# Performance work log

Hardware: AMD Instinct MI355X
Metric: run time of the kernel (lower is better)

The kernel has to match this reference:

```python
import jax, jax.numpy as jnp
import numpy as np
import math

H = 512        # hidden_dim
DEPTH = 5
KS = 3         # kernel size
DELTA = 0.1
M = 104        # timestamp == seq_len
NC = 5
B = 512
BN_EPS = 1e-5


def setup_inputs() -> dict:
    key = jax.random.key(0)
    ks = jax.random.split(key, 16)
    inp = {}
    inp['x'] = jax.random.normal(ks[0], (B, 1, M), dtype=jnp.float32)
    # CausalCNN: depth conv layers (first is 1->H, rest H->H), each followed by BN
    inp['conv_w0'] = jax.random.normal(ks[1], (H, 1, KS), dtype=jnp.float32) * (1.0 / np.sqrt(KS))
    inp['conv_b0'] = jnp.zeros((H,), jnp.float32)
    inp['conv_w'] = jax.random.normal(ks[2], (DEPTH - 1, H, H, KS), dtype=jnp.float32) * (1.0 / np.sqrt(H * KS))
    inp['conv_b'] = jnp.zeros((DEPTH - 1, H), jnp.float32)
    inp['bn_gamma'] = jnp.ones((DEPTH, H), jnp.float32)
    inp['bn_beta'] = jnp.zeros((DEPTH, H), jnp.float32)
    # input_proj
    inp['proj_w'] = jax.random.normal(ks[3], (H, H), dtype=jnp.float32) * (1.0 / np.sqrt(H))
    inp['proj_b'] = jnp.zeros((H,), jnp.float32)
    # ZOH layers: A = -0.01*I + 0.001*randn, B = 0.01*randn [H,1], C = 0.01*randn [1,H]
    eye = jnp.eye(H, dtype=jnp.float32)
    inp['A_all'] = -0.01 * eye[None] + 0.001 * jax.random.normal(ks[4], (DEPTH, H, H), dtype=jnp.float32)
    inp['B_all'] = 0.01 * jax.random.normal(ks[5], (DEPTH, H, 1), dtype=jnp.float32)
    inp['C_all'] = 0.01 * jax.random.normal(ks[6], (DEPTH, 1, H), dtype=jnp.float32)
    # fc_temp: Linear(H,H) -> BN1d(H) -> GELU -> Dropout(eval) -> Linear(H,NC)
    inp['fc1_w'] = jax.random.normal(ks[7], (H, H), dtype=jnp.float32) * (1.0 / np.sqrt(H))
    inp['fc1_b'] = jnp.zeros((H,), jnp.float32)
    inp['fc_bn_gamma'] = jnp.ones((H,), jnp.float32)
    inp['fc_bn_beta'] = jnp.zeros((H,), jnp.float32)
    inp['fc2_w'] = jax.random.normal(ks[8], (NC, H), dtype=jnp.float32) * (1.0 / np.sqrt(H))
    inp['fc2_b'] = jnp.zeros((NC,), jnp.float32)
    return inp


def _causal_conv(x, w, b):
    # x: [B, Cin, T], w: [Cout, Cin, K] -> left-pad K-1 (equivalent to pad both + trim right)
    y = jax.lax.conv_general_dilated(x, w, window_strides=(1,), padding=[(KS - 1, 0)],
                                     dimension_numbers=('NCH', 'OIH', 'NCH'))
    return y + b[None, :, None]


def _bn_ct(x, g, b):
    # BatchNorm1d over [B, C, T], batch statistics (training-mode normalization)
    m = x.mean(axis=(0, 2), keepdims=True)
    v = x.var(axis=(0, 2), keepdims=True)
    return g[None, :, None] * (x - m) * jax.lax.rsqrt(v + BN_EPS) + b[None, :, None]


def _pos_encoding(T, d):
    pos = jnp.arange(T, dtype=jnp.float32)[:, None]
    div = jnp.exp(jnp.arange(0, d, 2, dtype=jnp.float32) * (-math.log(10000.0) / d))
    pe = jnp.zeros((T, d), jnp.float32)
    pe = pe.at[:, 0::2].set(jnp.sin(pos * div))
    pe = pe.at[:, 1::2].set(jnp.cos(pos * div))
    return pe


def _zoh_kbar(A, Bv, Cv):
    # A: [H,H], Bv: [H,1], Cv: [1,H] -> normalized K_bar [M]
    A_bar = jax.scipy.linalg.expm(DELTA * A)
    I = jnp.eye(H, dtype=A.dtype)
    A_inv = jnp.linalg.inv(A + 0.001 * I)
    B_bar = A_inv @ (A_bar - I) @ (DELTA * Bv)  # [H,1]
    # term_k = C @ A_bar^k @ B_bar; sequential vector recurrence replaces matrix powers
    def step(v, _):
        term = (Cv @ v)[0, 0]
        return A_bar @ v, term
    _, terms = jax.lax.scan(step, B_bar, None, length=M)  # [M]
    Kb = jnp.flip(terms, axis=0)
    return Kb / (jnp.linalg.norm(Kb) + 1e-6)


def reference(x, conv_w0, conv_b0, conv_w, conv_b, bn_gamma, bn_beta, proj_w, proj_b,
              A_all, B_all, C_all, fc1_w, fc1_b, fc_bn_gamma, fc_bn_beta, fc2_w, fc2_b):
    # CausalCNN
    h = jax.nn.relu(_bn_ct(_causal_conv(x, conv_w0, conv_b0), bn_gamma[0], bn_beta[0]))
    for i in range(DEPTH - 1):
        h = jax.nn.relu(_bn_ct(_causal_conv(h, conv_w[i], conv_b[i]), bn_gamma[i + 1], bn_beta[i + 1]))
    h = jnp.transpose(h, (0, 2, 1))  # [B, T, H]
    # positional encoding + input projection
    h = h + _pos_encoding(M, H)[None]
    h = jnp.einsum('bth,oh->bto', h, proj_w) + proj_b
    # stacked ZOH kernels: each layer multiplies x by its normalized K_bar along time
    Ks = jax.vmap(_zoh_kbar)(A_all, B_all, C_all)  # [DEPTH, M]
    h = h * jnp.prod(Ks, axis=0)[None, :, None]
    # mean pool over time, then fc_temp (BN with batch stats, dropout = identity/eval)
    h = h.mean(axis=1)  # [B, H]
    h = jnp.dot(h, fc1_w.T) + fc1_b
    m = h.mean(axis=0, keepdims=True)
    v = h.var(axis=0, keepdims=True)
    h = fc_bn_gamma * (h - m) * jax.lax.rsqrt(v + BN_EPS) + fc_bn_beta
    h = jax.nn.gelu(h, approximate=False)
    logits = jnp.dot(h, fc2_w.T) + fc2_b  # [B, NC]
    return logits
```

## Files before the change

### kernel.cpp

```cpp
#include <hip/hip_runtime.h>
#include <cstdio>
#include <cmath>
#include <cstdint>

constexpr int BM = 512 * 104;
constexpr float BN_EPS = 1e-5f;

constexpr size_t SZ_BF   = (size_t)BM * 512 * 2;
constexpr size_t SZ_MAT5 = (size_t)5 * 512 * 512 * 4;
constexpr size_t OFF_YB0 = 0;
constexpr size_t OFF_YB1 = OFF_YB0 + SZ_BF;
constexpr size_t OFF_WT2 = OFF_YB1 + SZ_BF;
constexpr size_t OFF_X   = OFF_WT2 + 6291456;
constexpr size_t OFF_T1  = OFF_X   + SZ_MAT5;
constexpr size_t OFF_T2  = OFF_T1  + SZ_MAT5;
constexpr size_t OFF_E   = OFF_T2  + SZ_MAT5;
constexpr size_t OFF_MW  = OFF_E   + SZ_MAT5;
constexpr size_t OFF_P2  = OFF_MW  + SZ_MAT5;
constexpr size_t OFF_P4  = OFF_P2  + SZ_MAT5;
constexpr size_t OFF_ROWT= OFF_P4  + SZ_MAT5;
constexpr size_t OFF_COLS= OFF_ROWT + 655360;
constexpr size_t OFF_COLS2=OFF_COLS + 655360;
constexpr size_t OFF_PIVI= OFF_COLS2 + 655360;
constexpr size_t OFF_PJT = OFF_PIVI + 81920;
constexpr size_t OFF_F1T = OFF_PJT + 1048576;
constexpr size_t OFF_G   = OFF_F1T + 1048576;
constexpr size_t OFF_POOL= OFF_G   + 1048576;
constexpr size_t OFF_Z   = OFF_POOL + 1048576;
constexpr size_t OFF_ST  = OFF_Z   + 1048576;
constexpr size_t OFF_U   = OFF_ST  + 49152;
constexpr size_t OFF_SV  = OFF_U   + 10240;
constexpr size_t OFF_V   = OFF_SV  + 10240;
constexpr size_t OFF_WV  = OFF_V   + 81920;
constexpr size_t OFF_S   = OFF_WV  + 133120;
constexpr size_t WS_NEED = OFF_S + 512;

__device__ __forceinline__ float bf2f(unsigned short u) {
    union { uint32_t i; float f; } x; x.i = (uint32_t)u << 16; return x.f;
}
__device__ __forceinline__ unsigned short f2bf(float f) {
    union { float f; uint32_t i; } x; x.f = f;
    uint32_t r = x.i + 0x7FFFu + ((x.i >> 16) & 1u);
    return (unsigned short)(r >> 16);
}

typedef __bf16 bf16x8 __attribute__((ext_vector_type(8)));
typedef float  f32x4  __attribute__((ext_vector_type(4)));

__device__ __forceinline__ void gld16(const void* g, void* l) {
    __builtin_amdgcn_global_load_lds((const __attribute__((address_space(1))) uint32_t*)g,
                                     (__attribute__((address_space(3))) uint32_t*)l, 16, 0, 0);
}

__device__ __forceinline__ uint32_t bnrelu_pk(uint32_t u, float sc0, float sc1, float sh0, float sh1) {
    union { uint32_t i; float f; } a, b;
    a.i = u << 16;
    b.i = u & 0xFFFF0000u;
    float x0 = fmaxf(fmaf(a.f, sc0, sh0), 0.0f);
    float x1 = fmaxf(fmaf(b.f, sc1, sh1), 0.0f);
    uint32_t r;
    asm volatile("v_cvt_pk_bf16_f32 %0, %1, %2" : "=v"(r) : "v"(x0), "v"(x1));
    return r;
}

__global__ void k_build(const float* __restrict__ Aall, float* __restrict__ X, float* __restrict__ MW,
                        float* __restrict__ COLSa, const float* __restrict__ Call, float* __restrict__ WV)
{
    long i = (long)blockIdx.x * 256 + threadIdx.x;
    float a = Aall[i];
    X[i] = 0.1f * a;
    int z = (int)(i >> 18);
    int rc = (int)(i & 262143);
    int r = rc >> 9, c = rc & 511;
    float mw = a + ((r == c) ? 0.001f : 0.0f);
    MW[i] = mw;
    if (c < 64) COLSa[(long)z * 32768 + r * 64 + c] = mw;
    if (i < 2560) WV[(i >> 9) * 6656 + (i & 511)] = Call[i];
}

__global__ __launch_bounds__(256) void k_mm(
    const float* __restrict__ A, long sA, int lda,
    const float* __restrict__ Bm, long sB, int ldb,
    float* __restrict__ C, long sC, int ldc,
    int K, int mode,
    const float* __restrict__ aux, long sAux,
    const float* __restrict__ aux2, float* __restrict__ Cp,
    double* __restrict__ st1, double* __restrict__ st2, int pc)
{
    __shared__ float sm[2 * 32 * 68];
    float* As = sm;
    float* Bs = sm + 32 * 68;
    int z = blockIdx.z;
    A  += (long)z * sA;
    Bm += (long)z * sB;
    C  += (long)z * sC;
    if (aux) aux += (long)z * sAux;
    int m0 = blockIdx.x * 64, n0 = blockIdx.y * 64;
    int tid = threadIdx.x;
    int tx = tid & 15, ty = tid >> 4;
    float acc[4][4] = {};
    for (int k0 = 0; k0 < K; k0 += 32) {
        __syncthreads();
#pragma unroll
        for (int it = 0; it < 2; ++it) {
            int s = it * 256 + tid;
            int mm = s >> 3, k4 = (s & 7) * 4;
            float4 v = *(const float4*)&A[(long)(m0 + mm) * lda + k0 + k4];
            As[(k4 + 0) * 68 + mm] = v.x;
            As[(k4 + 1) * 68 + mm] = v.y;
            As[(k4 + 2) * 68 + mm] = v.z;
            As[(k4 + 3) * 68 + mm] = v.w;
        }
#pragma unroll
        for (int it = 0; it < 2; ++it) {
            int s = it * 256 + tid;
            int kk = s >> 4, n4 = (s & 15) * 4;
            *(float4*)&Bs[kk * 68 + n4] = *(const float4*)&Bm[(long)(k0 + kk) * ldb + n0 + n4];
        }
        __syncthreads();
#pragma unroll 8
        for (int kk = 0; kk < 32; ++kk) {
            float4 a = *(const float4*)&As[kk * 68 + ty * 4];
            float4 b = *(const float4*)&Bs[kk * 68 + tx * 4];
            float av[4] = {a.x, a.y, a.z, a.w};
            float bv[4] = {b.x, b.y, b.z, b.w};
#pragma unroll
            for (int i = 0; i < 4; ++i)
#pragma unroll
                for (int j = 0; j < 4; ++j)
                    acc[i][j] = fmaf(av[i], bv[j], acc[i][j]);
        }
    }
    float sc2 = (mode == 5) ? aux2[0] : 0.0f;
    float cs1[4] = {0, 0, 0, 0}, cs2[4] = {0, 0, 0, 0};
#pragma unroll
    for (int i = 0; i < 4; ++i) {
        int row = m0 + ty * 4 + i;
        int col0 = n0 + tx * 4;
        long base = (long)row * ldc + col0;
        float v[4];
#pragma unroll
        for (int j = 0; j < 4; ++j) v[j] = acc[i][j];
        if (mode == 1) {
            for (int j = 0; j < 4; ++j) {
                int col = col0 + j;
                v[j] = v[j] + 2.0f * aux[(long)row * 512 + col] + ((row == col) ? 1.0f : 0.0f);
            }
        } else if (mode == 2) {
            for (int j = 0; j < 4; ++j)
                v[j] = v[j] + aux[(long)row * 512 + col0 + j];
        } else if (mode == 3) {
            bool inP = (col0 >= pc && col0 < pc + 64);
            if (inP)
                for (int j = 0; j < 4; ++j) v[j] = aux[row * 64 + (col0 + j - pc)];
        } else if (mode == 5) {
            for (int j = 0; j < 4; ++j) v[j] += aux[col0 + j] * sc2;
        } else if (mode == 7) {
            float pv[4];
            for (int j = 0; j < 4; ++j) {
                int col = col0 + j;
                pv[j] = ((row == col) ? 0.5f : 0.0f) + aux[(long)row * 512 + col] * (1.0f / 6.0f)
                        + v[j] * (1.0f / 24.0f);
            }
            *(float4*)&Cp[base] = make_float4(pv[0], pv[1], pv[2], pv[3]);
        } else if (mode == 8) {
            for (int j = 0; j < 4; ++j) {
                v[j] += aux[col0 + j];
                cs1[j] += v[j]; cs2[j] += v[j] * v[j];
            }
        }
        *(float4*)&C[base] = make_float4(v[0], v[1], v[2], v[3]);
    }
    if (mode == 8) {
        __syncthreads();
        float* s1s = sm;
        float* s2s = sm + 1024;
#pragma unroll
        for (int j = 0; j < 4; ++j) {
            s1s[ty * 64 + tx * 4 + j] = cs1[j];
            s2s[ty * 64 + tx * 4 + j] = cs2[j];
        }
        __syncthreads();
        if (tid < 64) {
            double a = 0.0, b = 0.0;
#pragma unroll
            for (int t = 0; t < 16; ++t) { a += s1s[t * 64 + tid]; b += s2s[t * 64 + tid]; }
            atomicAdd(&st1[n0 + tid], a);
            atomicAdd(&st2[n0 + tid], b);
        }
    }
}

__global__ __launch_bounds__(256) void k_elim(
    const float* __restrict__ COLSc, const float* __restrict__ ROWT,
    float* __restrict__ MW, float* __restrict__ COLSn, int pr, int pcn)
{
    int z = blockIdx.z;
    COLSc += (long)z * 32768; ROWT += (long)z * 32768;
    MW += (long)z * 262144; COLSn += (long)z * 32768;
    int m0 = blockIdx.x * 64, n0 = blockIdx.y * 64;
    int tid = threadIdx.x;
    if (m0 == pr) {
        for (int it = 0; it < 16; ++it) {
            int idx = it * 256 + tid;
            int r = idx >> 6, c = idx & 63;
            float v = ROWT[r * 512 + n0 + c];
            MW[(long)(pr + r) * 512 + n0 + c] = v;
            if (n0 == pcn) COLSn[(pr + r) * 64 + c] = v;
        }
        return;
    }
    __shared__ float As[64 * 68];
    __shared__ float Bs[64 * 68];
    {
        int m = tid >> 2, kb = (tid & 3) * 16;
#pragma unroll
        for (int u = 0; u < 4; ++u) {
            float4 v = *(const float4*)&COLSc[(m0 + m) * 64 + kb + u * 4];
            As[(kb + u * 4 + 0) * 68 + m] = v.x;
            As[(kb + u * 4 + 1) * 68 + m] = v.y;
            As[(kb + u * 4 + 2) * 68 + m] = v.z;
            As[(kb + u * 4 + 3) * 68 + m] = v.w;
        }
        int kr = tid >> 2, nb = (tid & 3) * 16;
#pragma unroll
        for (int u = 0; u < 4; ++u)
            *(float4*)&Bs[kr * 68 + nb + u * 4] = *(const float4*)&ROWT[kr * 512 + n0 + nb + u * 4];
    }
    __syncthreads();
    int tx = tid & 15, ty = tid >> 4;
    float acc[4][4] = {};
#pragma unroll 8
    for (int kk = 0; kk < 64; ++kk) {
        float4 a = *(const float4*)&As[kk * 68 + ty * 4];
        float4 b = *(const float4*)&Bs[kk * 68 + tx * 4];
        float av[4] = {a.x, a.y, a.z, a.w};
        float bv[4] = {b.x, b.y, b.z, b.w};
#pragma unroll
        for (int i = 0; i < 4; ++i)
#pragma unroll
            for (int j = 0; j < 4; ++j)
                acc[i][j] = fmaf(av[i], bv[j], acc[i][j]);
    }
    bool inP = (n0 == pr);
#pragma unroll
    for (int i = 0; i < 4; ++i) {
        int row = m0 + ty * 4 + i;
        int col0 = n0 + tx * 4;
        long base = (long)row * 512 + col0;
        float ov[4] = {0.f, 0.f, 0.f, 0.f};
        if (!inP) {
            float4 oldv = *(const float4*)&MW[base];
            ov[0] = oldv.x; ov[1] = oldv.y; ov[2] = oldv.z; ov[3] = oldv.w;
        }
        float v[4];
#pragma unroll
        for (int j = 0; j < 4; ++j) v[j] = ov[j] - acc[i][j];
        *(float4*)&MW[base] = make_float4(v[0], v[1], v[2], v[3]);
        if (n0 == pcn)
            *(float4*)&COLSn[row * 64 + (col0 - pcn)] = make_float4(v[0], v[1], v[2], v[3]);
    }
}

__global__ __launch_bounds__(256) void k_inv64(float* __restrict__ MW, int pblk, float* __restrict__ PIVI)
{
    __shared__ float mat[64 * 65];
    __shared__ float fv[64];
    __shared__ int perm[64];
    __shared__ int arr[64];
    __shared__ int pividx;
    __shared__ float dv;
    int z = blockIdx.x;
    float* Mg = MW + (long)z * 262144 + (long)pblk * 64 * 512 + pblk * 64;
    int tid = threadIdx.x;
    for (int it = 0; it < 16; ++it) {
        int idx = it * 256 + tid;
        int r = idx >> 6, c = idx & 63;
        mat[r * 65 + c] = Mg[r * 512 + c];
    }
    __syncthreads();
    for (int j = 0; j < 64; ++j) {
        if (tid < 64) {
            float v = (tid >= j) ? fabsf(mat[tid * 65 + j]) : -1.0f;
            int idx = tid;
#pragma unroll
            for (int off = 32; off; off >>= 1) {
                float ov = __shfl_down(v, off);
                int oi = __shfl_down(idx, off);
                if (ov > v) { v = ov; idx = oi; }
            }
            if (tid == 0) pividx = idx;
        }
        __syncthreads();
        int r = pividx;
        if (tid < 64) {
            if (r != j) {
                float tj = mat[j * 65 + tid], tr = mat[r * 65 + tid];
                mat[j * 65 + tid] = tr; mat[r * 65 + tid] = tj;
            }
            if (tid == 0) perm[j] = r;
        }
        __syncthreads();
        if (tid < 64) {
            float piv = mat[j * 65 + j];
            float d = 1.0f / piv;
            fv[tid] = mat[tid * 65 + j];
            mat[j * 65 + tid] = (tid == j) ? d : mat[j * 65 + tid] * d;
            if (tid == 0) dv = d;
        }
        __syncthreads();
        {
            int i = tid & 63, c0 = (tid >> 6) * 16;
            if (i != j) {
                float f = fv[i];
                float dd = dv;
#pragma unroll
                for (int u = 0; u < 16; ++u) {
                    int c = c0 + u;
                    float val = mat[i * 65 + c] - f * mat[j * 65 + c];
                    if (c == j) val = -f * dd;
                    mat[i * 65 + c] = val;
                }
            }
        }
        __syncthreads();
    }
    if (tid == 0) {
        for (int c = 0; c < 64; ++c) arr[c] = c;
        for (int j = 63; j >= 0; --j) { int r = perm[j]; int t = arr[j]; arr[j] = arr[r]; arr[r] = t; }
    }
    __syncthreads();
    float* Pg = PIVI + z * 4096;
    for (int it = 0; it < 16; ++it) {
        int idx = it * 256 + tid;
        int r = idx >> 6, c = idx & 63;
        Pg[r * 64 + c] = mat[r * 65 + arr[c]];
    }
}

__global__ void k_matvecA(const float* __restrict__ A, long sA,
                          const float* __restrict__ x, long sx,
                          float* __restrict__ y, long sy,
                          const float* __restrict__ sub, long ssub,
                          float alpha, float beta, int accum)
{
    int row = blockIdx.x, z = blockIdx.y, lane = threadIdx.x;
    A += (long)z * sA; x += (long)z * sx; y += (long)z * sy;
    if (sub) sub += (long)z * ssub;
    const float* ar = A + (long)row * 512;
    double acc = 0.0;
#pragma unroll
    for (int m = 0; m < 8; ++m) {
        int k = lane + m * 64;
        acc += (double)ar[k] * (double)x[k];
    }
    for (int off = 32; off; off >>= 1) acc += __shfl_down(acc, off);
    if (lane == 0) {
        float val = alpha * (float)acc + beta * x[row];
        if (sub) val = sub[row] - val;
        if (accum) y[row] += val; else y[row] = val;
    }
}

struct VWT { long a[8]; long x[8]; long y[8]; float al[8]; float be[8]; int ty[8]; };
__global__ void k_vw(const char* __restrict__ ws, VWT T)
{
    int g = blockIdx.x, z = blockIdx.y, t = blockIdx.z;
    int lane = threadIdx.x;
    const float* A = (const float*)(ws + T.a[t]) + (long)z * 262144;
    int ty = T.ty[t];
    long vs = ty ? 6656 : 4096;
    const float* x = (const float*)(ws + T.x[t]) + (long)z * vs;
    float* yv = (float*)(ws + T.y[t]) + (long)z * vs;
    if (ty == 0) {
        float xm[8];
#pragma unroll
        for (int m = 0; m < 8; ++m) xm[m] = x[lane + m * 64];
        float alpha = T.al[t], beta = T.be[t];
        for (int r0 = 0; r0 < 64; ++r0) {
            int row = g * 64 + r0;
            const float* ar = A + (long)row * 512;
            double acc = 0.0;
#pragma unroll
            for (int m = 0; m < 8; ++m) acc += (double)ar[lane + m * 64] * (double)xm[m];
            for (int off = 32; off; off >>= 1) acc += __shfl_down(acc, off);
            if (lane == 0) yv[row] = alpha * (float)acc + beta * x[row];
        }
    } else {
        __shared__ float xl[512];
#pragma unroll
        for (int m = 0; m < 8; ++m) xl[lane + m * 64] = x[lane + m * 64];
        __syncthreads();
        int c = g * 64 + lane;
        double acc = 0.0;
#pragma unroll 8
        for (int j = 0; j < 512; ++j) acc += (double)A[(long)j * 512 + c] * (double)xl[j];
        yv[c] = (float)acc;
    }
}

__global__ __launch_bounds__(512) void k_termsk(const float* __restrict__ WV, const float* __restrict__ V,
                                                float* __restrict__ svec)
{
    __shared__ float tl[520];
    __shared__ float invn[5];
    __shared__ float red[2];
    int tid = threadIdx.x;
    for (int t = tid; t < 520; t += 512) {
        int z = t / 104, d = t - z * 104;
        int j = d >> 3, i = d & 7;
        const float* wp = WV + z * 6656 + j * 512;
        const float* vp = V + z * 4096 + i * 512;
        float acc = 0.0f;
#pragma unroll 8
        for (int k = 0; k < 512; ++k) acc += wp[k] * vp[k];
        tl[t] = acc;
    }
    __syncthreads();
    int w = tid >> 6, lane = tid & 63;
    if (w < 5) {
        float a = tl[w * 104 + lane]; a = a * a;
        if (lane < 40) { float b = tl[w * 104 + 64 + lane]; a += b * b; }
#pragma unroll
        for (int off = 32; off; off >>= 1) a += __shfl_down(a, off);
        if (lane == 0) invn[w] = 1.0f / (sqrtf(a) + 1e-6f);
    }
    __syncthreads();
    float s = 0.0f;
    if (tid < 104) {
        s = 1.0f;
        for (int l = 0; l < 5; ++l) s *= tl[l * 104 + (103 - tid)] * invn[l];
        svec[tid] = s;
    }
    if (tid < 128) {
        float v = (tid < 104) ? s : 0.0f;
#pragma unroll
        for (int off = 32; off; off >>= 1) v += __shfl_down(v, off);
        if ((tid & 63) == 0) red[tid >> 6] = v;
    }
    __syncthreads();
    if (tid == 0) svec[104] = (red[0] + red[1]) * (1.0f / 104.0f);
}

__global__ void k_conv0(const float* __restrict__ x, const float* __restrict__ w0, const float* __restrict__ b0,
                        unsigned short* __restrict__ y, double* __restrict__ s1g, double* __restrict__ s2g)
{
    int b = blockIdx.x;
    int c = blockIdx.y * 256 + threadIdx.x;
    float w_0 = w0[c * 3 + 0], w_1 = w0[c * 3 + 1], w_2 = w0[c * 3 + 2], bb = b0[c];
    const float* xb = x + b * 104;
    unsigned short* yb = y + (long)b * 104 * 512 + c;
    float xm2 = 0.0f, xm1 = 0.0f;
    float s1 = 0.0f, s2 = 0.0f;
    for (int t = 0; t < 104; ++t) {
        float x0 = xb[t];
        float v = w_0 * xm2 + w_1 * xm1 + w_2 * x0 + bb;
        yb[t * 512] = f2bf(v);
        s1 += v; s2 += v * v;
        xm2 = xm1; xm1 = x0;
    }
    atomicAdd(&s1g[c], (double)s1);
    atomicAdd(&s2g[c], (double)s2);
}

__global__ void k_wt2(const float* __restrict__ W, unsigned short* __restrict__ Wt2)
{
    int co = blockIdx.x, l = blockIdx.y, tid = threadIdx.x;
    const float* src = W + (long)(l * 512 + co) * 512 * 3;
    unsigned short* dst = Wt2 + (long)l * 3 * 262144 + ((long)co << 9);
    int v = (co >> 1) & 3;
#pragma unroll
    for (int q = 0; q < 2; ++q) {
        int ci = tid * 2 + q;
        int chunk = (ci >> 3) & 3;
        int di = (ci & ~31) + (((chunk ^ v) & 3) << 3) + (ci & 7);
        float f0 = src[ci * 3 + 0], f1 = src[ci * 3 + 1], f2 = src[ci * 3 + 2];
        dst[di] = f2bf(f0);
        dst[262144 + di] = f2bf(f1);
        dst[524288 + di] = f2bf(f2);
    }
}

__global__ __launch_bounds__(256, 2) void k_convm(
    const unsigned short* __restrict__ act,
    const unsigned short* __restrict__ Wt2,
    const float* __restrict__ bias,
    const double* __restrict__ STin,
    const float* __restrict__ gam, const float* __restrict__ bet,
    unsigned short* __restrict__ yout,
    double* __restrict__ s1g, double* __restrict__ s2g)
{
    __shared__ __align__(16) unsigned short As[130 * 32];
    __shared__ __align__(16) unsigned short Bs[3 * 256 * 32];
    __shared__ float SCs[512];
    __shared__ float SHs[512];
    int tid = threadIdx.x;
    int m0 = blockIdx.x * 128, co0 = blockIdx.y * 256;
    int w = tid >> 6, lane = tid & 63;
    int wr = (w >> 1) * 64, wc = (w & 1) * 128;
    int fr = lane & 15, quad = lane >> 4;

    const double invN = 1.0 / (double)BM;
    for (int c = tid; c < 512; c += 256) {
        double mn = STin[c] * invN;
        double var = STin[512 + c] * invN - mn * mn;
        double rs = 1.0 / sqrt(var + (double)BN_EPS);
        double scd = (double)gam[c] * rs;
        SCs[c] = (float)scd;
        SHs[c] = (float)((double)bet[c] - mn * scd);
    }

    bool valid[4][3];
#pragma unroll
    for (int i = 0; i < 4; ++i) {
        int R = m0 + wr + i * 16 + fr;
        int t = R % 104;
#pragma unroll
        for (int tau = 0; tau < 3; ++tau) valid[i][tau] = (t + tau >= 2);
    }

    int aoff[4][3];
#pragma unroll
    for (int i = 0; i < 4; ++i)
#pragma unroll
        for (int tau = 0; tau < 3; ++tau) {
            int r = wr + i * 16 + fr + tau;
            aoff[i][tau] = r * 32 + (((quad ^ (r >> 1)) & 3) << 3);
        }
    int boff[8];
#pragma unroll
    for (int j = 0; j < 8; ++j) {
        int rb = wc + j * 16 + fr;
        boff[j] = rb * 32 + (((quad ^ (rb >> 1)) & 3) << 3);
    }

    int ka = (tid & 3) * 8;
    int g0 = m0 - 2 + (tid >> 2); if (g0 < 0) g0 = 0;
    int g1 = m0 + 62 + (tid >> 2);
    int g2 = m0 + 126 + (tid >> 2);
    const unsigned short* pa0 = act + (long)g0 * 512 + ka;
    const unsigned short* pa1 = act + (long)g1 * 512 + ka;
    const unsigned short* pa2 = act + (long)g2 * 512 + ka;
    int wbase = (tid >> 2) * 32 + ((((tid & 3) ^ (tid >> 3)) & 3) << 3);
    const unsigned short* pbB = Wt2 + ((long)(co0 + (tid >> 2)) << 9) + ka;

    f32x4 zero4 = {0.f, 0.f, 0.f, 0.f};
    f32x4 acc[4][8];
#pragma unroll
    for (int i = 0; i < 4; ++i)
#pragma unroll
        for (int j = 0; j < 8; ++j) acc[i][j] = zero4;
    bf16x8 zer = {0, 0, 0, 0, 0, 0, 0, 0};

#pragma unroll 1
    for (int s = 0; s < 16; ++s) {
        int ci0 = s * 32;
        __syncthreads();
        uint4 va0 = *(const uint4*)(pa0 + ci0);
        uint4 va1 = *(const uint4*)(pa1 + ci0);
        uint4 va2;
        if (tid < 8) va2 = *(const uint4*)(pa2 + ci0);
#pragma unroll
        for (int tau = 0; tau < 3; ++tau)
#pragma unroll
            for (int it = 0; it < 4; ++it)
                gld16(pbB + tau * 262144 + it * 32768 + ci0, &Bs[(tau * 4 + it) * 2048 + tid * 8]);
        int cb = ci0 + ka;
        float4 s0 = *(const float4*)&SCs[cb], s1v = *(const float4*)&SCs[cb + 4];
        float4 h0 = *(const float4*)&SHs[cb], h1v = *(const float4*)&SHs[cb + 4];
        {
            uint4 pk;
            pk.x = bnrelu_pk(va0.x, s0.x, s0.y, h0.x, h0.y);
            pk.y = bnrelu_pk(va0.y, s0.z, s0.w, h0.z, h0.w);
            pk.z = bnrelu_pk(va0.z, s1v.x, s1v.y, h1v.x, h1v.y);
            pk.w = bnrelu_pk(va0.w, s1v.z, s1v.w, h1v.z, h1v.w);
            *(uint4*)&As[wbase] = pk;
            pk.x = bnrelu_pk(va1.x, s0.x, s0.y, h0.x, h0.y);
            pk.y = bnrelu_pk(va1.y, s0.z, s0.w, h0.z, h0.w);
            pk.z = bnrelu_pk(va1.z, s1v.x, s1v.y, h1v.x, h1v.y);
            pk.w = bnrelu_pk(va1.w, s1v.z, s1v.w, h1v.z, h1v.w);
            *(uint4*)&As[wbase + 2048] = pk;
            if (tid < 8) {
                pk.x = bnrelu_pk(va2.x, s0.x, s0.y, h0.x, h0.y);
                pk.y = bnrelu_pk(va2.y, s0.z, s0.w, h0.z, h0.w);
                pk.z = bnrelu_pk(va2.z, s1v.x, s1v.y, h1v.x, h1v.y);
                pk.w = bnrelu_pk(va2.w, s1v.z, s1v.w, h1v.z, h1v.w);
                *(uint4*)&As[wbase + 4096] = pk;
            }
        }
        __syncthreads();
#pragma unroll
        for (int tau = 0; tau < 3; ++tau) {
            bf16x8 af[4];
#pragma unroll
            for (int i = 0; i < 4; ++i) {
                bf16x8 raw = *(const bf16x8*)&As[aoff[i][tau]];
                af[i] = valid[i][tau] ? raw : zer;
            }
            bf16x8 bfr[8];
#pragma unroll
            for (int j = 0; j < 8; ++j)
                bfr[j] = *(const bf16x8*)&Bs[tau * 8192 + boff[j]];
#pragma unroll
            for (int i = 0; i < 4; ++i)
#pragma unroll
                for (int j = 0; j < 8; ++j)
                    acc[i][j] = __builtin_amdgcn_mfma_f32_16x16x32_bf16(af[i], bfr[j], acc[i][j], 0, 0, 0);
        }
    }
    float bcol[8], s1[8], s2[8];
#pragma unroll
    for (int jt = 0; jt < 8; ++jt) {
        bcol[jt] = bias[co0 + wc + jt * 16 + fr];
        s1[jt] = 0.0f; s2[jt] = 0.0f;
    }
#pragma unroll
    for (int i = 0; i < 4; ++i) {
        int rbase = m0 + wr + i * 16 + quad * 4;
#pragma unroll
        for (int jt = 0; jt < 8; ++jt) {
            int col = co0 + wc + jt * 16 + fr;
#pragma unroll
            for (int r = 0; r < 4; ++r) {
                float v = acc[i][jt][r] + bcol[jt];
                yout[(long)(rbase + r) * 512 + col] = f2bf(v);
                s1[jt] += v; s2[jt] += v * v;
            }
        }
    }
#pragma unroll
    for (int jt = 0; jt < 8; ++jt) {
        s1[jt] += __shfl_xor(s1[jt], 16); s1[jt] += __shfl_xor(s1[jt], 32);
        s2[jt] += __shfl_xor(s2[jt], 16); s2[jt] += __shfl_xor(s2[jt], 32);
    }
    __syncthreads();
    float* st = (float*)As;
    if (lane < 16) {
#pragma unroll
        for (int jt = 0; jt < 8; ++jt) {
            st[w * 128 + jt * 16 + lane] = s1[jt];
            st[512 + w * 128 + jt * 16 + lane] = s2[jt];
        }
    }
    __syncthreads();
    {
        int half = tid >> 7, cl = tid & 127;
        float a = st[half * 128 + cl] + st[(half + 2) * 128 + cl];
        float b = st[512 + half * 128 + cl] + st[512 + (half + 2) * 128 + cl];
        atomicAdd(&s1g[co0 + tid], (double)a);
        atomicAdd(&s2g[co0 + tid], (double)b);
    }
}

__global__ void k_pool(const unsigned short* __restrict__ y4, const double* __restrict__ ST4,
                       const float* __restrict__ gam, const float* __restrict__ bet,
                       const float* __restrict__ svec, float* __restrict__ g)
{
    __shared__ float sl[104];
    int b = blockIdx.x;
    int c = blockIdx.y * 256 + threadIdx.x;
    if (threadIdx.x < 104) sl[threadIdx.x] = svec[threadIdx.x];
    __syncthreads();
    const double invN = 1.0 / (double)BM;
    double mn = ST4[c] * invN;
    double var = ST4[512 + c] * invN - mn * mn;
    double rs = 1.0 / sqrt(var + (double)BN_EPS);
    double scd = (double)gam[c] * rs;
    float sc = (float)scd, sh = (float)((double)bet[c] - mn * scd);
    int he = c & ~1;
    float div = expf((float)he * (-0.017988946039015984f));
    float acc = 0.0f;
    const unsigned short* yb = y4 + (long)b * 104 * 512 + c;
    for (int t = 0; t < 104; ++t) {
        float v = bf2f(yb[t * 512]);
        float hn = fmaxf(fmaf(v, sc, sh), 0.0f);
        float arg = (float)t * div;
        float pe = (c & 1) ? cosf(arg) : sinf(arg);
        acc += sl[t] * (hn + pe);
    }
    g[(long)b * 512 + c] = acc * (1.0f / 104.0f);
}

__global__ void k_t512(const float* __restrict__ in0, float* __restrict__ out0,
                       const float* __restrict__ in1, float* __restrict__ out1)
{
    __shared__ float tile[64 * 68];
    const float* in = blockIdx.z ? in1 : in0;
    float* outp = blockIdx.z ? out1 : out0;
    int bx = blockIdx.x, by = blockIdx.y;
    int tid = threadIdx.x;
    for (int it = 0; it < 4; ++it) {
        int s = it * 256 + tid;
        int r = s >> 4, c4 = (s & 15) * 4;
        *(float4*)&tile[r * 68 + c4] = *(const float4*)&in[(long)(bx * 64 + r) * 512 + by * 64 + c4];
    }
    __syncthreads();
    for (int it = 0; it < 4; ++it) {
        int s = it * 256 + tid;
        int r = s >> 4, c4 = (s & 15) * 4;
        float4 v;
        v.x = tile[(c4 + 0) * 68 + r];
        v.y = tile[(c4 + 1) * 68 + r];
        v.z = tile[(c4 + 2) * 68 + r];
        v.w = tile[(c4 + 3) * 68 + r];
        *(float4*)&outp[(long)(by * 64 + r) * 512 + bx * 64 + c4] = v;
    }
}

__global__ __launch_bounds__(256) void k_final(const float* __restrict__ zin, const double* __restrict__ st,
                                               const float* __restrict__ gam, const float* __restrict__ bet,
                                               const float* __restrict__ w2, const float* __restrict__ b2,
                                               float* __restrict__ outp)
{
    __shared__ float red[256];
    int b = blockIdx.x, tid = threadIdx.x;
    int oo[2] = { tid, tid + 256 };
    float gv[2];
#pragma unroll
    for (int q = 0; q < 2; ++q) {
        int o = oo[q];
        double m = st[o] * (1.0 / 512.0);
        double var = st[512 + o] * (1.0 / 512.0) - m * m;
        double rs = 1.0 / sqrt(var + (double)BN_EPS);
        float xn = (float)(((double)zin[(long)b * 512 + o] - m) * rs * (double)gam[o] + (double)bet[o]);
        gv[q] = 0.5f * xn * (1.0f + erff(xn * 0.70710678118654752f));
    }
    for (int n = 0; n < 5; ++n) {
        float p = gv[0] * w2[n * 512 + oo[0]] + gv[1] * w2[n * 512 + oo[1]];
        red[tid] = p;
        __syncthreads();
        for (int off = 128; off; off >>= 1) { if (tid < off) red[tid] += red[tid + off]; __syncthreads(); }
        if (tid == 0) outp[b * 5 + n] = red[0] + b2[n];
        __syncthreads();
    }
}

static void mm(hipStream_t s, int Mt, int Nt, int z,
               const float* A, long sA, int lda,
               const float* B, long sB, int ldb,
               float* C, long sC, int ldc,
               int K, int mode,
               const float* aux = nullptr, long sAux = 0, const float* aux2 = nullptr,
               float* Cp = nullptr, double* st1 = nullptr, double* st2 = nullptr, int pc = 0)
{
    dim3 g(Mt, Nt, z);
    k_mm<<<g, 256, 0, s>>>(A, sA, lda, B, sB, ldb, C, sC, ldc, K, mode, aux, sAux, aux2, Cp, st1, st2, pc);
}

extern "C" void kernel_launch(void* const* d_in, const int* in_sizes, int n_in,
                              void* d_out, int out_size, void* d_ws, size_t ws_size,
                              hipStream_t stream)
{
    (void)in_sizes; (void)n_in; (void)out_size;
    const float* x       = (const float*)d_in[0];
    const float* conv_w0 = (const float*)d_in[1];
    const float* conv_b0 = (const float*)d_in[2];
    const float* conv_w  = (const float*)d_in[3];
    const float* conv_b  = (const float*)d_in[4];
    const float* bn_g    = (const float*)d_in[5];
    const float* bn_b    = (const float*)d_in[6];
    const float* proj_w  = (const float*)d_in[7];
    const float* proj_b  = (const float*)d_in[8];
    const float* A_all   = (const float*)d_in[9];
    const float* B_all   = (const float*)d_in[10];
    const float* C_all   = (const float*)d_in[11];
    const float* fc1_w   = (const float*)d_in[12];
    const float* fc1_b   = (const float*)d_in[13];
    const float* fbn_g   = (const float*)d_in[14];
    const float* fbn_b   = (const float*)d_in[15];
    const float* fc2_w   = (const float*)d_in[16];
    const float* fc2_b   = (const float*)d_in[17];
    float* outp = (float*)d_out;
    char* ws = (char*)d_ws;
    if (ws_size < WS_NEED) { printf("ws too small: %zu < %zu\n", ws_size, WS_NEED); return; }

    unsigned short* YB0 = (unsigned short*)(ws + OFF_YB0);
    unsigned short* YB1 = (unsigned short*)(ws + OFF_YB1);
    unsigned short* WT2 = (unsigned short*)(ws + OFF_WT2);
    float* Xb   = (float*)(ws + OFF_X);
    float* T1   = (float*)(ws + OFF_T1);
    float* T2   = (float*)(ws + OFF_T2);
    float* Eb   = (float*)(ws + OFF_E);
    float* MW   = (float*)(ws + OFF_MW);
    float* P2   = (float*)(ws + OFF_P2);
    float* P4   = (float*)(ws + OFF_P4);
    float* ROWT = (float*)(ws + OFF_ROWT);
    float* COLS1= (float*)(ws + OFF_COLS);
    float* COLS2= (float*)(ws + OFF_COLS2);
    float* PIVI = (float*)(ws + OFF_PIVI);
    float* PJT  = (float*)(ws + OFF_PJT);
    float* F1T  = (float*)(ws + OFF_F1T);
    float* G    = (float*)(ws + OFF_G);
    float* POOL = (float*)(ws + OFF_POOL);
    float* Zb   = (float*)(ws + OFF_Z);
    double* ST  = (double*)(ws + OFF_ST);
    float* U    = (float*)(ws + OFF_U);
    float* SV   = (float*)(ws + OFF_SV);
    float* V    = (float*)(ws + OFF_V);
    float* WV   = (float*)(ws + OFF_WV);
    float* SVEC = (float*)(ws + OFF_S);

    const long SM = 262144;
    hipMemsetAsync(ws + OFF_ST, 0, 49152, stream);

    k_wt2<<<dim3(512, 4), 256, 0, stream>>>(conv_w, WT2);
    k_build<<<5120, 256, 0, stream>>>(A_all, Xb, MW, COLS1, C_all, WV);
    for (int p = 0; p < 8; ++p) {
        int pc = p * 64;
        float* Cc = (p & 1) ? COLS2 : COLS1;
        float* Cn = (p & 1) ? COLS1 : COLS2;
        k_inv64<<<5, 256, 0, stream>>>(MW, p, PIVI);
        mm(stream, 1, 8, 5, PIVI, 4096, 64, MW + pc * 512, SM, 512, ROWT, 32768, 512, 64, 3,
           PIVI, 4096, nullptr, nullptr, nullptr, nullptr, pc);
        k_elim<<<dim3(8, 8, 5), 256, 0, stream>>>(Cc, ROWT, MW, Cn, pc, pc + 64);
    }
    mm(stream, 8, 8, 5, Xb, SM, 512, Xb, SM, 512, T2, SM, 512, 512, 7, Xb, SM, nullptr, T1);
    mm(stream, 8, 8, 5, T2, SM, 512, T1, SM, 512, Eb, SM, 512, 512, 2, Xb, SM);
    mm(stream, 8, 8, 5, Eb, SM, 512, Eb, SM, 512, Xb, SM, 512, 512, 1, Eb, SM);
    mm(stream, 8, 8, 5, Xb, SM, 512, Xb, SM, 512, T1, SM, 512, 512, 0);
    mm(stream, 8, 8, 5, T1, SM, 512, T1, SM, 512, T2, SM, 512, 512, 0);
    mm(stream, 8, 8, 5, T2, SM, 512, T2, SM, 512, P2, SM, 512, 512, 0);
    mm(stream, 8, 8, 5, P2, SM, 512, P2, SM, 512, P4, SM, 512, 512, 0);
    k_matvecA<<<dim3(512, 5), 64, 0, stream>>>(Eb, SM, B_all, 512, U, 512, nullptr, 0, 0.1f, 0.0f, 0);
    k_matvecA<<<dim3(512, 5), 64, 0, stream>>>(MW, SM, U, 512, V, 4096, nullptr, 0, 1.0f, 0.0f, 0);
    k_matvecA<<<dim3(512, 5), 64, 0, stream>>>(A_all, SM, V, 4096, SV, 512, U, 512, 1.0f, 0.001f, 0);
    k_matvecA<<<dim3(512, 5), 64, 0, stream>>>(MW, SM, SV, 512, V, 4096, nullptr, 0, 1.0f, 0.0f, 1);
    auto Voff = [](int i) { return (long)(OFF_V + (size_t)i * 2048); };
    auto Woff = [](int j) { return (long)(OFF_WV + (size_t)j * 2048); };
    {
        VWT T = {};
        T.a[0] = OFF_E;  T.x[0] = Voff(0); T.y[0] = Voff(1); T.al[0] = 1; T.be[0] = 1; T.ty[0] = 0;
        T.a[1] = OFF_T2; T.x[1] = Woff(0); T.y[1] = Woff(1); T.ty[1] = 1;
        k_vw<<<dim3(8, 5, 2), 64, 0, stream>>>(ws, T);
    }
    {
        VWT T = {};
        T.a[0] = OFF_X;  T.x[0] = Voff(0); T.y[0] = Voff(2); T.al[0] = 1; T.ty[0] = 0;
        T.a[1] = OFF_X;  T.x[1] = Voff(1); T.y[1] = Voff(3); T.al[1] = 1; T.ty[1] = 0;
        T.a[2] = OFF_P2; T.x[2] = Woff(0); T.y[2] = Woff(2); T.ty[2] = 1;
        T.a[3] = OFF_P2; T.x[3] = Woff(1); T.y[3] = Woff(3); T.ty[3] = 1;
        k_vw<<<dim3(8, 5, 4), 64, 0, stream>>>(ws, T);
    }
    {
        VWT T = {};
        for (int i = 0; i < 4; ++i) {
            T.a[i] = OFF_T1; T.x[i] = Voff(i); T.y[i] = Voff(4 + i); T.al[i] = 1; T.ty[i] = 0;
            T.a[4 + i] = OFF_P4; T.x[4 + i] = Woff(i); T.y[4 + i] = Woff(4 + i); T.ty[4 + i] = 1;
        }
        k_vw<<<dim3(8, 5, 8), 64, 0, stream>>>(ws, T);
    }
    {
        VWT T = {};
        for (int i = 0; i < 4; ++i) {
            T.a[i] = OFF_P4; T.x[i] = Woff(4 + i); T.y[i] = Woff(8 + i); T.ty[i] = 1;
        }
        k_vw<<<dim3(8, 5, 4), 64, 0, stream>>>(ws, T);
    }
    {
        VWT T = {};
        T.a[0] = OFF_P4; T.x[0] = Woff(8); T.y[0] = Woff(12); T.ty[0] = 1;
        k_vw<<<dim3(8, 5, 1), 64, 0, stream>>>(ws, T);
    }
    k_termsk<<<1, 512, 0, stream>>>(WV, V, SVEC);

    k_conv0<<<dim3(512, 2), 256, 0, stream>>>(x, conv_w0, conv_b0, YB0, ST, ST + 512);
    for (int l = 1; l <= 4; ++l) {
        unsigned short* inb  = (l & 1) ? YB0 : YB1;
        unsigned short* outb = (l & 1) ? YB1 : YB0;
        k_convm<<<dim3(416, 2), 256, 0, stream>>>(inb, WT2 + (size_t)(l - 1) * 3 * 262144,
                                                  conv_b + (l - 1) * 512,
                                                  ST + (l - 1) * 1024, bn_g + (l - 1) * 512, bn_b + (l - 1) * 512,
                                                  outb, ST + l * 1024, ST + l * 1024 + 512);
    }
    k_pool<<<dim3(512, 2), 256, 0, stream>>>(YB0, ST + 4 * 1024, bn_g + 4 * 512, bn_b + 4 * 512, SVEC, G);

    k_t512<<<dim3(8, 8, 2), 256, 0, stream>>>(proj_w, PJT, fc1_w, F1T);
    mm(stream, 8, 8, 1, G, 0, 512, PJT, 0, 512, POOL, 0, 512, 512, 5, proj_b, 0, SVEC + 104);
    mm(stream, 8, 8, 1, POOL, 0, 512, F1T, 0, 512, Zb, 0, 512, 512, 8, fc1_b, 0, nullptr, nullptr,
       ST + 5 * 1024, ST + 5 * 1024 + 512);
    k_final<<<512, 256, 0, stream>>>(Zb, ST + 5 * 1024, fbn_g, fbn_b, fc2_w, fc2_b, outp);
}
```

Measured before the change: 1.809 ms.

## Fuse block-inverse row update into elimination, merge weight prep and matvec chain

The blocked Gauss-Jordan inversion loop now computes the pivot-row product inside a single elimination kernel, using ping-pong matrix buffers (MW/P2), so the separate per-step GEMM launch is gone. The conv-weight transpose kernel is merged with the ZOH build kernel into one launch, and the four chained matvec launches become one kernel per layer that keeps the intermediate vectors in shared memory. Together these cut the launch count in the serial setup chain. In exchange, each elimination block redoes the 64x64 row product, and the matvec stage now runs on only 5 blocks, so it uses far less of the GPU.

```diff
diff --git a/kernel.cpp b/kernel.cpp
--- a/kernel.cpp
+++ b/kernel.cpp
@@ -63,10 +63,30 @@
     return r;
 }
 
-__global__ void k_build(const float* __restrict__ Aall, float* __restrict__ X, float* __restrict__ MW,
-                        float* __restrict__ COLSa, const float* __restrict__ Call, float* __restrict__ WV)
-{
-    long i = (long)blockIdx.x * 256 + threadIdx.x;
+__global__ void k_bw(const float* __restrict__ W, unsigned short* __restrict__ Wt2,
+                     const float* __restrict__ Aall, float* __restrict__ X, float* __restrict__ MW,
+                     float* __restrict__ COLSa, const float* __restrict__ Call, float* __restrict__ WV)
+{
+    int bid = blockIdx.x;
+    int tid = threadIdx.x;
+    if (bid < 2048) {
+        int co = bid & 511, l = bid >> 9;
+        const float* src = W + (long)(l * 512 + co) * 512 * 3;
+        unsigned short* dst = Wt2 + (long)l * 3 * 262144 + ((long)co << 9);
+        int v = (co >> 1) & 3;
+#pragma unroll
+        for (int q = 0; q < 2; ++q) {
+            int ci = tid * 2 + q;
+            int chunk = (ci >> 3) & 3;
+            int di = (ci & ~31) + (((chunk ^ v) & 3) << 3) + (ci & 7);
+            float f0 = src[ci * 3 + 0], f1 = src[ci * 3 + 1], f2 = src[ci * 3 + 2];
+            dst[di] = f2bf(f0);
+            dst[262144 + di] = f2bf(f1);
+            dst[524288 + di] = f2bf(f2);
+        }
+        return;
+    }
+    long i = (long)(bid - 2048) * 256 + tid;
     float a = Aall[i];
     X[i] = 0.1f * a;
     int z = (int)(i >> 18);
@@ -149,10 +169,6 @@
         } else if (mode == 2) {
             for (int j = 0; j < 4; ++j)
                 v[j] = v[j] + aux[(long)row * 512 + col0 + j];
-        } else if (mode == 3) {
-            bool inP = (col0 >= pc && col0 < pc + 64);
-            if (inP)
-                for (int j = 0; j < 4; ++j) v[j] = aux[row * 64 + (col0 + j - pc)];
         } else if (mode == 5) {
             for (int j = 0; j < 4; ++j) v[j] += aux[col0 + j] * sc2;
         } else if (mode == 7) {
@@ -191,27 +207,77 @@
     }
 }
 
-__global__ __launch_bounds__(256) void k_elim(
-    const float* __restrict__ COLSc, const float* __restrict__ ROWT,
-    float* __restrict__ MW, float* __restrict__ COLSn, int pr, int pcn)
-{
+__global__ __launch_bounds__(256) void k_elim2(
+    const float* __restrict__ MWin, float* __restrict__ MWout,
+    const float* __restrict__ PIVI, const float* __restrict__ COLSc,
+    float* __restrict__ COLSn, int pc, int pcn)
+{
+    __shared__ float As[64 * 68];
+    __shared__ float Rs[64 * 68];
     int z = blockIdx.z;
-    COLSc += (long)z * 32768; ROWT += (long)z * 32768;
-    MW += (long)z * 262144; COLSn += (long)z * 32768;
+    MWin += (long)z * 262144; MWout += (long)z * 262144;
+    PIVI += z * 4096; COLSc += (long)z * 32768; COLSn += (long)z * 32768;
     int m0 = blockIdx.x * 64, n0 = blockIdx.y * 64;
     int tid = threadIdx.x;
-    if (m0 == pr) {
+    int tx = tid & 15, ty = tid >> 4;
+
+    if (n0 == pc) {
         for (int it = 0; it < 16; ++it) {
             int idx = it * 256 + tid;
             int r = idx >> 6, c = idx & 63;
-            float v = ROWT[r * 512 + n0 + c];
-            MW[(long)(pr + r) * 512 + n0 + c] = v;
-            if (n0 == pcn) COLSn[(pr + r) * 64 + c] = v;
+            Rs[r * 68 + c] = PIVI[r * 64 + c];
+        }
+        __syncthreads();
+    } else {
+        {
+            int m = tid >> 2, kb = (tid & 3) * 16;
+#pragma unroll
+            for (int u = 0; u < 4; ++u) {
+                float4 v = *(const float4*)&PIVI[m * 64 + kb + u * 4];
+                As[(kb + u * 4 + 0) * 68 + m] = v.x;
+                As[(kb + u * 4 + 1) * 68 + m] = v.y;
+                As[(kb + u * 4 + 2) * 68 + m] = v.z;
+                As[(kb + u * 4 + 3) * 68 + m] = v.w;
+            }
+            int kr = tid >> 2, cb = (tid & 3) * 16;
+#pragma unroll
+            for (int u = 0; u < 4; ++u)
+                *(float4*)&Rs[kr * 68 + cb + u * 4] =
+                    *(const float4*)&MWin[(long)(pc + kr) * 512 + n0 + cb + u * 4];
+        }
+        __syncthreads();
+        float acc1[4][4] = {};
+#pragma unroll 8
+        for (int kk = 0; kk < 64; ++kk) {
+            float4 a = *(const float4*)&As[kk * 68 + ty * 4];
+            float4 b = *(const float4*)&Rs[kk * 68 + tx * 4];
+            float av[4] = {a.x, a.y, a.z, a.w};
+            float bv[4] = {b.x, b.y, b.z, b.w};
+#pragma unroll
+            for (int i = 0; i < 4; ++i)
+#pragma unroll
+                for (int j = 0; j < 4; ++j)
+                    acc1[i][j] = fmaf(av[i], bv[j], acc1[i][j]);
+        }
+        __syncthreads();
+#pragma unroll
+        for (int i = 0; i < 4; ++i)
+#pragma unroll
+            for (int j = 0; j < 4; ++j)
+                Rs[(ty * 4 + i) * 68 + tx * 4 + j] = acc1[i][j];
+        __syncthreads();
+    }
+
+    if (m0 == pc) {
+        for (int it = 0; it < 16; ++it) {
+            int idx = it * 256 + tid;
+            int r = idx >> 6, c = idx & 63;
+            float v = Rs[r * 68 + c];
+            MWout[(long)(pc + r) * 512 + n0 + c] = v;
+            if (n0 == pcn) COLSn[(pc + r) * 64 + c] = v;
         }
         return;
     }
-    __shared__ float As[64 * 68];
-    __shared__ float Bs[64 * 68];
     {
         int m = tid >> 2, kb = (tid & 3) * 16;
 #pragma unroll
@@ -222,18 +288,13 @@
             As[(kb + u * 4 + 2) * 68 + m] = v.z;
             As[(kb + u * 4 + 3) * 68 + m] = v.w;
         }
-        int kr = tid >> 2, nb = (tid & 3) * 16;
-#pragma unroll
-        for (int u = 0; u < 4; ++u)
-            *(float4*)&Bs[kr * 68 + nb + u * 4] = *(const float4*)&ROWT[kr * 512 + n0 + nb + u * 4];
-    }
-    __syncthreads();
-    int tx = tid & 15, ty = tid >> 4;
+    }
+    __syncthreads();
     float acc[4][4] = {};
 #pragma unroll 8
     for (int kk = 0; kk < 64; ++kk) {
         float4 a = *(const float4*)&As[kk * 68 + ty * 4];
-        float4 b = *(const float4*)&Bs[kk * 68 + tx * 4];
+        float4 b = *(const float4*)&Rs[kk * 68 + tx * 4];
         float av[4] = {a.x, a.y, a.z, a.w};
         float bv[4] = {b.x, b.y, b.z, b.w};
 #pragma unroll
@@ -242,7 +303,7 @@
             for (int j = 0; j < 4; ++j)
                 acc[i][j] = fmaf(av[i], bv[j], acc[i][j]);
     }
-    bool inP = (n0 == pr);
+    bool inP = (n0 == pc);
 #pragma unroll
     for (int i = 0; i < 4; ++i) {
         int row = m0 + ty * 4 + i;
@@ -250,19 +311,19 @@
         long base = (long)row * 512 + col0;
         float ov[4] = {0.f, 0.f, 0.f, 0.f};
         if (!inP) {
-            float4 oldv = *(const float4*)&MW[base];
+            float4 oldv = *(const float4*)&MWin[base];
             ov[0] = oldv.x; ov[1] = oldv.y; ov[2] = oldv.z; ov[3] = oldv.w;
         }
         float v[4];
 #pragma unroll
         for (int j = 0; j < 4; ++j) v[j] = ov[j] - acc[i][j];
-        *(float4*)&MW[base] = make_float4(v[0], v[1], v[2], v[3]);
+        *(float4*)&MWout[base] = make_float4(v[0], v[1], v[2], v[3]);
         if (n0 == pcn)
             *(float4*)&COLSn[row * 64 + (col0 - pcn)] = make_float4(v[0], v[1], v[2], v[3]);
     }
 }
 
-__global__ __launch_bounds__(256) void k_inv64(float* __restrict__ MW, int pblk, float* __restrict__ PIVI)
+__global__ __launch_bounds__(256) void k_inv64(const float* __restrict__ MW, int pblk, float* __restrict__ PIVI)
 {
     __shared__ float mat[64 * 65];
     __shared__ float fv[64];
@@ -271,7 +332,7 @@
     __shared__ int pividx;
     __shared__ float dv;
     int z = blockIdx.x;
-    float* Mg = MW + (long)z * 262144 + (long)pblk * 64 * 512 + pblk * 64;
+    const float* Mg = MW + (long)z * 262144 + (long)pblk * 64 * 512 + pblk * 64;
     int tid = threadIdx.x;
     for (int it = 0; it < 16; ++it) {
         int idx = it * 256 + tid;
@@ -338,27 +399,55 @@
     }
 }
 
-__global__ void k_matvecA(const float* __restrict__ A, long sA,
-                          const float* __restrict__ x, long sx,
-                          float* __restrict__ y, long sy,
-                          const float* __restrict__ sub, long ssub,
-                          float alpha, float beta, int accum)
-{
-    int row = blockIdx.x, z = blockIdx.y, lane = threadIdx.x;
-    A += (long)z * sA; x += (long)z * sx; y += (long)z * sy;
-    if (sub) sub += (long)z * ssub;
-    const float* ar = A + (long)row * 512;
-    double acc = 0.0;
-#pragma unroll
-    for (int m = 0; m < 8; ++m) {
-        int k = lane + m * 64;
-        acc += (double)ar[k] * (double)x[k];
-    }
-    for (int off = 32; off; off >>= 1) acc += __shfl_down(acc, off);
-    if (lane == 0) {
-        float val = alpha * (float)acc + beta * x[row];
-        if (sub) val = sub[row] - val;
-        if (accum) y[row] += val; else y[row] = val;
+__global__ __launch_bounds__(1024) void k_bbar(const float* __restrict__ Eb, const float* __restrict__ MW,
+                                               const float* __restrict__ Aall, const float* __restrict__ Ball,
+                                               float* __restrict__ V)
+{
+    __shared__ float xs[512], us[512], vs[512], sv[512];
+    int z = blockIdx.x;
+    const float* E  = Eb   + (long)z * 262144;
+    const float* Mi = MW   + (long)z * 262144;
+    const float* Aa = Aall + (long)z * 262144;
+    int tid = threadIdx.x, lane = tid & 63, w = tid >> 6;
+    if (tid < 512) xs[tid] = Ball[z * 512 + tid];
+    __syncthreads();
+    for (int r = w * 32; r < w * 32 + 32; ++r) {
+        const float* ar = E + (long)r * 512;
+        double acc = 0.0;
+#pragma unroll
+        for (int m = 0; m < 8; ++m) acc += (double)ar[lane + m * 64] * (double)xs[lane + m * 64];
+        for (int off = 32; off; off >>= 1) acc += __shfl_down(acc, off);
+        if (lane == 0) us[r] = 0.1f * (float)acc;
+    }
+    __syncthreads();
+    for (int r = w * 32; r < w * 32 + 32; ++r) {
+        const float* ar = Mi + (long)r * 512;
+        double acc = 0.0;
+#pragma unroll
+        for (int m = 0; m < 8; ++m) acc += (double)ar[lane + m * 64] * (double)us[lane + m * 64];
+        for (int off = 32; off; off >>= 1) acc += __shfl_down(acc, off);
+        if (lane == 0) vs[r] = 1.0f * (float)acc;
+    }
+    __syncthreads();
+    for (int r = w * 32; r < w * 32 + 32; ++r) {
+        const float* ar = Aa + (long)r * 512;
+        double acc = 0.0;
+#pragma unroll
+        for (int m = 0; m < 8; ++m) acc += (double)ar[lane + m * 64] * (double)vs[lane + m * 64];
+        for (int off = 32; off; off >>= 1) acc += __shfl_down(acc, off);
+        if (lane == 0) {
+            float val = 1.0f * (float)acc + 0.001f * vs[r];
+            sv[r] = us[r] - val;
+        }
+    }
+    __syncthreads();
+    for (int r = w * 32; r < w * 32 + 32; ++r) {
+        const float* ar = Mi + (long)r * 512;
+        double acc = 0.0;
+#pragma unroll
+        for (int m = 0; m < 8; ++m) acc += (double)ar[lane + m * 64] * (double)sv[lane + m * 64];
+        for (int off = 32; off; off >>= 1) acc += __shfl_down(acc, off);
+        if (lane == 0) V[(long)z * 4096 + r] = vs[r] + 1.0f * (float)acc;
     }
 }
 
@@ -461,24 +550,6 @@
     }
     atomicAdd(&s1g[c], (double)s1);
     atomicAdd(&s2g[c], (double)s2);
-}
-
-__global__ void k_wt2(const float* __restrict__ W, unsigned short* __restrict__ Wt2)
-{
-    int co = blockIdx.x, l = blockIdx.y, tid = threadIdx.x;
-    const float* src = W + (long)(l * 512 + co) * 512 * 3;
-    unsigned short* dst = Wt2 + (long)l * 3 * 262144 + ((long)co << 9);
-    int v = (co >> 1) & 3;
-#pragma unroll
-    for (int q = 0; q < 2; ++q) {
-        int ci = tid * 2 + q;
-        int chunk = (ci >> 3) & 3;
-        int di = (ci & ~31) + (((chunk ^ v) & 3) << 3) + (ci & 7);
-        float f0 = src[ci * 3 + 0], f1 = src[ci * 3 + 1], f2 = src[ci * 3 + 2];
-        dst[di] = f2bf(f0);
-        dst[262144 + di] = f2bf(f1);
-        dst[524288 + di] = f2bf(f2);
-    }
 }
 
 __global__ __launch_bounds__(256, 2) void k_convm(
@@ -784,7 +855,6 @@
     float* MW   = (float*)(ws + OFF_MW);
     float* P2   = (float*)(ws + OFF_P2);
     float* P4   = (float*)(ws + OFF_P4);
-    float* ROWT = (float*)(ws + OFF_ROWT);
     float* COLS1= (float*)(ws + OFF_COLS);
     float* COLS2= (float*)(ws + OFF_COLS2);
     float* PIVI = (float*)(ws + OFF_PIVI);
@@ -794,8 +864,6 @@
     float* POOL = (float*)(ws + OFF_POOL);
     float* Zb   = (float*)(ws + OFF_Z);
     double* ST  = (double*)(ws + OFF_ST);
-    float* U    = (float*)(ws + OFF_U);
-    float* SV   = (float*)(ws + OFF_SV);
     float* V    = (float*)(ws + OFF_V);
     float* WV   = (float*)(ws + OFF_WV);
     float* SVEC = (float*)(ws + OFF_S);
@@ -803,16 +871,19 @@
     const long SM = 262144;
     hipMemsetAsync(ws + OFF_ST, 0, 49152, stream);
 
-    k_wt2<<<dim3(512, 4), 256, 0, stream>>>(conv_w, WT2);
-    k_build<<<5120, 256, 0, stream>>>(A_all, Xb, MW, COLS1, C_all, WV);
-    for (int p = 0; p < 8; ++p) {
-        int pc = p * 64;
-        float* Cc = (p & 1) ? COLS2 : COLS1;
-        float* Cn = (p & 1) ? COLS1 : COLS2;
-        k_inv64<<<5, 256, 0, stream>>>(MW, p, PIVI);
-        mm(stream, 1, 8, 5, PIVI, 4096, 64, MW + pc * 512, SM, 512, ROWT, 32768, 512, 64, 3,
-           PIVI, 4096, nullptr, nullptr, nullptr, nullptr, pc);
-        k_elim<<<dim3(8, 8, 5), 256, 0, stream>>>(Cc, ROWT, MW, Cn, pc, pc + 64);
+    k_bw<<<7168, 256, 0, stream>>>(conv_w, WT2, A_all, Xb, MW, COLS1, C_all, WV);
+
+    {
+        float* MB[2] = { MW, P2 };
+        for (int p = 0; p < 8; ++p) {
+            int pc = p * 64;
+            float* Mi = MB[p & 1];
+            float* Mo = MB[(p + 1) & 1];
+            float* Cc = (p & 1) ? COLS2 : COLS1;
+            float* Cn = (p & 1) ? COLS1 : COLS2;
+            k_inv64<<<5, 256, 0, stream>>>(Mi, p, PIVI);
+            k_elim2<<<dim3(8, 8, 5), 256, 0, stream>>>(Mi, Mo, PIVI, Cc, Cn, pc, pc + 64);
+        }
     }
     mm(stream, 8, 8, 5, Xb, SM, 512, Xb, SM, 512, T2, SM, 512, 512, 7, Xb, SM, nullptr, T1);
     mm(stream, 8, 8, 5, T2, SM, 512, T1, SM, 512, Eb, SM, 512, 512, 2, Xb, SM);
@@ -821,10 +892,7 @@
     mm(stream, 8, 8, 5, T1, SM, 512, T1, SM, 512, T2, SM, 512, 512, 0);
     mm(stream, 8, 8, 5, T2, SM, 512, T2, SM, 512, P2, SM, 512, 512, 0);
     mm(stream, 8, 8, 5, P2, SM, 512, P2, SM, 512, P4, SM, 512, 512, 0);
-    k_matvecA<<<dim3(512, 5), 64, 0, stream>>>(Eb, SM, B_all, 512, U, 512, nullptr, 0, 0.1f, 0.0f, 0);
-    k_matvecA<<<dim3(512, 5), 64, 0, stream>>>(MW, SM, U, 512, V, 4096, nullptr, 0, 1.0f, 0.0f, 0);
-    k_matvecA<<<dim3(512, 5), 64, 0, stream>>>(A_all, SM, V, 4096, SV, 512, U, 512, 1.0f, 0.001f, 0);
-    k_matvecA<<<dim3(512, 5), 64, 0, stream>>>(MW, SM, SV, 512, V, 4096, nullptr, 0, 1.0f, 0.0f, 1);
+    k_bbar<<<5, 1024, 0, stream>>>(Eb, MW, A_all, B_all, V);
     auto Voff = [](int i) { return (long)(OFF_V + (size_t)i * 2048); };
     auto Woff = [](int j) { return (long)(OFF_WV + (size_t)j * 2048); };
     {
```

After: 1.834 ms. Within noise of the previous version (+1.4%).
